# Kernel optimization log

Hardware: AMD Instinct MI355X
Metric: run time of the kernel (lower is better)

## Reference

```python
import jax, jax.numpy as jnp
import numpy as np

EPS = 1e-8


def setup_inputs() -> dict:
    key = jax.random.key(0)
    k1, k2 = jax.random.split(key)
    x = jax.random.normal(k1, (32, 16, 4096), dtype=jnp.float32)
    # shapelets param: (in_channels, num_shapelets, shapelets_size)
    shapelets = jax.random.normal(k2, (16, 64, 64), dtype=jnp.float32)
    return {"x": x, "shapelets": shapelets}


def reference(x, shapelets):
    # x: (B, C, L); shapelets: (C, K, S)
    S = shapelets.shape[2]
    C = x.shape[1]
    W = x.shape[2] - S + 1
    # sliding windows, equivalent to torch unfold(2, S, 1): (B, C, W, S)
    idx = jnp.arange(W)[:, None] + jnp.arange(S)[None, :]
    win = x[:, :, idx]
    win = win / jnp.maximum(jnp.linalg.norm(win, axis=3, keepdims=True), EPS)
    sh = shapelets / jnp.maximum(jnp.linalg.norm(shapelets, axis=2, keepdims=True), EPS)
    # pairwise cosine dot, then mean over channels: (B, W, K)
    sim = jnp.einsum('bcws,cks->bwk', win, sh) / C
    # relu then global max over window positions; torch keeps the summed dim -> (B, 1, K)
    out = jnp.max(jax.nn.relu(sim), axis=1)[:, None, :]
    return out
```

## Files before the change

kernel.cpp:

```cpp
#include <hip/hip_runtime.h>

typedef unsigned int u32;
typedef unsigned short u16;
typedef __bf16 bf16x8 __attribute__((ext_vector_type(8)));
typedef float f32x4 __attribute__((ext_vector_type(4)));

static __device__ __forceinline__ u16 f2bf(float f) {
  u32 u = __float_as_uint(f);
  return (u16)((u + 0x7fffu + ((u >> 16) & 1u)) >> 16);
}
static __device__ __forceinline__ float b2f(u16 v) {
  return __uint_as_float(((u32)v) << 16);
}
static __device__ __forceinline__ u32 pk2(u16 lo, u16 hi) {
  return (u32)lo | ((u32)hi << 16);
}

__global__ __launch_bounds__(256) void prep_kernel(const float* __restrict__ sh,
                                                   u16* __restrict__ shn2,
                                                   float* __restrict__ out) {
  if (blockIdx.x == 0) {
    float4 z = {0.f, 0.f, 0.f, 0.f};
    *(float4*)&out[threadIdx.x * 8] = z;
    *(float4*)&out[threadIdx.x * 8 + 4] = z;
  }
  const int s = threadIdx.x & 63;
  const int wv = threadIdx.x >> 6;
  const int row0 = blockIdx.x * 16 + wv * 4;
#pragma unroll
  for (int r = 0; r < 4; ++r) {
    const int row = row0 + r;
    float v = sh[row * 64 + s];
    float ss = v * v;
#pragma unroll
    for (int o = 1; o < 64; o <<= 1) ss += __shfl_xor(ss, o, 64);
    float iw = 1.0f / fmaxf(sqrtf(ss), 1e-8f);
    const int c = row >> 6, k = row & 63;
    const int chunk = c * 8 + (k >> 4) * 2 + (s >> 5);
    const int pos = ((k & 15) + (((s & 31) >> 3) << 4)) * 8 + (s & 7);
    shn2[chunk * 512 + pos] = f2bf(v * iw);
  }
}

#define WT 128
#define CSTRIDE 104
#define SSTRIDE 1672

__global__ __launch_bounds__(256, 4) void main_kernel(const float* __restrict__ x,
                                                      const u16* __restrict__ shn2,
                                                      float* __restrict__ out) {
  __shared__ u32 xs[4 * SSTRIDE];
  __shared__ u16 invwb[16 * WT];
  __shared__ int redbuf[64];

  const int tid = threadIdx.x;
  const int lane = tid & 63;
  const int wid = tid >> 6;
  const int w0 = blockIdx.x * WT;
  const int b = blockIdx.y;
  const float* xb = x + (size_t)b * 16 * 4096;

  if (tid < 64) redbuf[tid] = 0;

  {
    const int q = tid & 15;
    const int c = tid >> 4;
    if (q < 12) {
      const float* xc = xb + c * 4096;
      const int e0 = w0 + 16 * q;
      float xv[20];
      if (e0 + 19 < 4096) {
#pragma unroll
        for (int r = 0; r < 5; ++r) *(float4*)&xv[4 * r] = *(const float4*)&xc[e0 + 4 * r];
      } else {
#pragma unroll
        for (int j = 0; j < 20; ++j) {
          int g = e0 + j;
          xv[j] = xc[g < 4096 ? g : 4095];
        }
      }
      u16 bf[20];
#pragma unroll
      for (int j = 0; j < 20; ++j) bf[j] = f2bf(xv[j]);
#pragma unroll
      for (int s = 0; s < 4; ++s) {
        u32 pk[8];
#pragma unroll
        for (int r = 0; r < 8; ++r) pk[r] = pk2(bf[2 * r + s], bf[2 * r + s + 1]);
        u32* dst = &xs[s * SSTRIDE + c * CSTRIDE + 8 * q];
        *(uint4*)dst = make_uint4(pk[0], pk[1], pk[2], pk[3]);
        *(uint4*)(dst + 4) = make_uint4(pk[4], pk[5], pk[6], pk[7]);
      }
    }
  }

  {
    const int c = tid >> 4;
    const int wb = (tid & 15) * 8;
    const float* xc = xb + c * 4096;
    const int e0 = w0 + wb;
    float hd[8], tl[8], ss = 0.f;
    if (e0 + 71 < 4096) {
#pragma unroll
      for (int r = 0; r < 16; ++r) {
        float4 v = *(const float4*)&xc[e0 + 4 * r];
        if (r < 2) {
          hd[4 * r + 0] = v.x; hd[4 * r + 1] = v.y;
          hd[4 * r + 2] = v.z; hd[4 * r + 3] = v.w;
        }
        ss += v.x * v.x + v.y * v.y + v.z * v.z + v.w * v.w;
      }
#pragma unroll
      for (int r = 0; r < 2; ++r) {
        float4 v = *(const float4*)&xc[e0 + 64 + 4 * r];
        tl[4 * r + 0] = v.x; tl[4 * r + 1] = v.y;
        tl[4 * r + 2] = v.z; tl[4 * r + 3] = v.w;
      }
    } else {
#pragma unroll
      for (int j = 0; j < 72; ++j) {
        int g = e0 + j;
        float v = xc[g < 4096 ? g : 4095];
        if (j < 8) hd[j] = v;
        if (j >= 64) tl[j - 64] = v;
        if (j < 64) ss += v * v;
      }
    }
    u16 ov[8];
#pragma unroll
    for (int i = 0; i < 8; ++i) {
      float iw = 0.0625f / fmaxf(sqrtf(fmaxf(ss, 0.f)), 1e-8f);
      ov[i] = (e0 + i < 4033) ? f2bf(iw) : (u16)0;
      ss += tl[i] * tl[i] - hd[i] * hd[i];
    }
    *(uint4*)&invwb[c * WT + wb] = make_uint4(pk2(ov[0], ov[1]), pk2(ov[2], ov[3]),
                                              pk2(ov[4], ov[5]), pk2(ov[6], ov[7]));
  }

  __syncthreads();

  f32x4 acc[4][2];
#pragma unroll
  for (int mt = 0; mt < 4; ++mt)
#pragma unroll
    for (int nt = 0; nt < 2; ++nt) acc[mt][nt] = (f32x4){0.f, 0.f, 0.f, 0.f};

  const int m = lane & 15;
  const int h = lane >> 4;
  const int wgrp = wid >> 1;
  const int kgrp = wid & 1;
  const u32* xbase = xs + (m & 3) * SSTRIDE;
  const int joff = 32 * wgrp + 2 * (m >> 2) + 4 * h;
  const u16* shb = shn2 + lane * 8 + kgrp * 4 * 512;
  const int iwbase = 64 * wgrp + 4 * h;

#pragma unroll 2
  for (int c = 0; c < 16; ++c) {
    const u32* xc = xbase + c * CSTRIDE;
    bf16x8 af[6];
#pragma unroll
    for (int f = 0; f < 6; ++f) {
      const u32* p = xc + joff + 8 * f;
      uint2 lo = *(const uint2*)p;
      uint2 hi = *(const uint2*)(p + 2);
      af[f] = __builtin_bit_cast(bf16x8, make_uint4(lo.x, lo.y, hi.x, hi.y));
    }
    const u16* sc = shb + c * 4096;
    bf16x8 bfr[2][2];
#pragma unroll
    for (int nt = 0; nt < 2; ++nt)
#pragma unroll
      for (int ks = 0; ks < 2; ++ks)
        bfr[nt][ks] = __builtin_bit_cast(bf16x8, *(const uint4*)(sc + (nt * 2 + ks) * 512));

#pragma unroll
    for (int mt = 0; mt < 4; ++mt) {
      ushort4 r4 = *(const ushort4*)&invwb[c * WT + iwbase + 16 * mt];
      f32x4 iw = {b2f(r4.x), b2f(r4.y), b2f(r4.z), b2f(r4.w)};
#pragma unroll
      for (int nt = 0; nt < 2; ++nt) {
        f32x4 d = {0.f, 0.f, 0.f, 0.f};
        d = __builtin_amdgcn_mfma_f32_16x16x32_bf16(af[mt],     bfr[nt][0], d, 0, 0, 0);
        d = __builtin_amdgcn_mfma_f32_16x16x32_bf16(af[mt + 2], bfr[nt][1], d, 0, 0, 0);
        acc[mt][nt] += iw * d;
      }
    }
  }

#pragma unroll
  for (int nt = 0; nt < 2; ++nt) {
    float v = 0.f;
#pragma unroll
    for (int mt = 0; mt < 4; ++mt)
      v = fmaxf(v, fmaxf(fmaxf(acc[mt][nt].x, acc[mt][nt].y),
                         fmaxf(acc[mt][nt].z, acc[mt][nt].w)));
    v = fmaxf(v, __shfl_xor(v, 16, 64));
    v = fmaxf(v, __shfl_xor(v, 32, 64));
    if (lane < 16) atomicMax(&redbuf[kgrp * 32 + nt * 16 + lane], __float_as_int(v));
  }
  __syncthreads();
  if (tid < 64) atomicMax((int*)&out[b * 64 + tid], redbuf[tid]);
}

extern "C" void kernel_launch(void* const* d_in, const int* in_sizes, int n_in,
                              void* d_out, int out_size, void* d_ws, size_t ws_size,
                              hipStream_t stream) {
  const float* x = (const float*)d_in[0];
  const float* sh = (const float*)d_in[1];
  float* out = (float*)d_out;
  u16* shn2 = (u16*)d_ws;

  prep_kernel<<<dim3(64), dim3(256), 0, stream>>>(sh, shn2, out);
  main_kernel<<<dim3(32, 32), dim3(256), 0, stream>>>(x, shn2, out);
}
```

Baseline: 45.03 us.

## Double window tile per block and give each wave all 64 shapelets

Each block now covers 256 window positions instead of 128, and each wave computes all 64 shapelets over its 64 windows rather than splitting shapelets across two waves. This halves the grid and the redundant halo loads and norm work per window, and it reuses the A fragments across four N tiles. The cost is twice the accumulator registers, a larger LDS footprint, lower occupancy (launch bounds 3) and fewer blocks, 512 of them across the GPU's compute units.

```diff
diff --git a/kernel.cpp b/kernel.cpp
--- a/kernel.cpp
+++ b/kernel.cpp
@@ -42,15 +42,16 @@
   }
 }
 
-#define WT 128
-#define CSTRIDE 104
-#define SSTRIDE 1672
-
-__global__ __launch_bounds__(256, 4) void main_kernel(const float* __restrict__ x,
+#define WT 256
+#define CSTRIDE 168
+#define SSTRIDE 2696
+#define IWS 264
+
+__global__ __launch_bounds__(256, 3) void main_kernel(const float* __restrict__ x,
                                                       const u16* __restrict__ shn2,
                                                       float* __restrict__ out) {
   __shared__ u32 xs[4 * SSTRIDE];
-  __shared__ u16 invwb[16 * WT];
+  __shared__ u16 invwb[16 * IWS];
   __shared__ int redbuf[64];
 
   const int tid = threadIdx.x;
@@ -63,96 +64,97 @@
   if (tid < 64) redbuf[tid] = 0;
 
   {
+    const int c = tid >> 4;
     const int q = tid & 15;
-    const int c = tid >> 4;
-    if (q < 12) {
-      const float* xc = xb + c * 4096;
-      const int e0 = w0 + 16 * q;
-      float xv[20];
-      if (e0 + 19 < 4096) {
-#pragma unroll
-        for (int r = 0; r < 5; ++r) *(float4*)&xv[4 * r] = *(const float4*)&xc[e0 + 4 * r];
-      } else {
-#pragma unroll
-        for (int j = 0; j < 20; ++j) {
-          int g = e0 + j;
-          xv[j] = xc[g < 4096 ? g : 4095];
-        }
-      }
-      u16 bf[20];
-#pragma unroll
-      for (int j = 0; j < 20; ++j) bf[j] = f2bf(xv[j]);
-#pragma unroll
-      for (int s = 0; s < 4; ++s) {
-        u32 pk[8];
-#pragma unroll
-        for (int r = 0; r < 8; ++r) pk[r] = pk2(bf[2 * r + s], bf[2 * r + s + 1]);
-        u32* dst = &xs[s * SSTRIDE + c * CSTRIDE + 8 * q];
-        *(uint4*)dst = make_uint4(pk[0], pk[1], pk[2], pk[3]);
-        *(uint4*)(dst + 4) = make_uint4(pk[4], pk[5], pk[6], pk[7]);
+    const float* xc = xb + c * 4096;
+    const int e0 = w0 + 20 * q;
+    float xv[24];
+    if (e0 + 23 < 4096) {
+#pragma unroll
+      for (int r = 0; r < 6; ++r) *(float4*)&xv[4 * r] = *(const float4*)&xc[e0 + 4 * r];
+    } else {
+#pragma unroll
+      for (int j = 0; j < 24; ++j) {
+        int g = e0 + j;
+        xv[j] = xc[g < 4096 ? g : 4095];
+      }
+    }
+    u16 bf[24];
+#pragma unroll
+    for (int j = 0; j < 24; ++j) bf[j] = f2bf(xv[j]);
+#pragma unroll
+    for (int s = 0; s < 4; ++s) {
+      u32* dst = &xs[s * SSTRIDE + c * CSTRIDE + 10 * q];
+#pragma unroll
+      for (int r = 0; r < 5; ++r) {
+        uint2 v = make_uint2(pk2(bf[4 * r + s], bf[4 * r + s + 1]),
+                             pk2(bf[4 * r + s + 2], bf[4 * r + s + 3]));
+        *(uint2*)(dst + 2 * r) = v;
       }
     }
   }
 
   {
     const int c = tid >> 4;
-    const int wb = (tid & 15) * 8;
+    const int wb = (tid & 15) * 16;
     const float* xc = xb + c * 4096;
     const int e0 = w0 + wb;
-    float hd[8], tl[8], ss = 0.f;
-    if (e0 + 71 < 4096) {
+    float hd[16], tl[16], ss = 0.f;
+    if (e0 + 79 < 4096) {
 #pragma unroll
       for (int r = 0; r < 16; ++r) {
         float4 v = *(const float4*)&xc[e0 + 4 * r];
-        if (r < 2) {
+        if (r < 4) {
           hd[4 * r + 0] = v.x; hd[4 * r + 1] = v.y;
           hd[4 * r + 2] = v.z; hd[4 * r + 3] = v.w;
         }
         ss += v.x * v.x + v.y * v.y + v.z * v.z + v.w * v.w;
       }
 #pragma unroll
-      for (int r = 0; r < 2; ++r) {
+      for (int r = 0; r < 4; ++r) {
         float4 v = *(const float4*)&xc[e0 + 64 + 4 * r];
         tl[4 * r + 0] = v.x; tl[4 * r + 1] = v.y;
         tl[4 * r + 2] = v.z; tl[4 * r + 3] = v.w;
       }
     } else {
 #pragma unroll
-      for (int j = 0; j < 72; ++j) {
+      for (int j = 0; j < 80; ++j) {
         int g = e0 + j;
         float v = xc[g < 4096 ? g : 4095];
-        if (j < 8) hd[j] = v;
+        if (j < 16) hd[j] = v;
         if (j >= 64) tl[j - 64] = v;
         if (j < 64) ss += v * v;
       }
     }
-    u16 ov[8];
-#pragma unroll
-    for (int i = 0; i < 8; ++i) {
+    u16 ov[16];
+#pragma unroll
+    for (int i = 0; i < 16; ++i) {
       float iw = 0.0625f / fmaxf(sqrtf(fmaxf(ss, 0.f)), 1e-8f);
       ov[i] = (e0 + i < 4033) ? f2bf(iw) : (u16)0;
       ss += tl[i] * tl[i] - hd[i] * hd[i];
     }
-    *(uint4*)&invwb[c * WT + wb] = make_uint4(pk2(ov[0], ov[1]), pk2(ov[2], ov[3]),
-                                              pk2(ov[4], ov[5]), pk2(ov[6], ov[7]));
+    u32* dst = (u32*)&invwb[c * IWS + wb];
+    *(uint4*)dst = make_uint4(pk2(ov[0], ov[1]), pk2(ov[2], ov[3]),
+                              pk2(ov[4], ov[5]), pk2(ov[6], ov[7]));
+    *(uint4*)(dst + 4) = make_uint4(pk2(ov[8], ov[9]), pk2(ov[10], ov[11]),
+                                    pk2(ov[12], ov[13]), pk2(ov[14], ov[15]));
   }
 
   __syncthreads();
 
-  f32x4 acc[4][2];
+  f32x4 acc[4][4];
 #pragma unroll
   for (int mt = 0; mt < 4; ++mt)
 #pragma unroll
-    for (int nt = 0; nt < 2; ++nt) acc[mt][nt] = (f32x4){0.f, 0.f, 0.f, 0.f};
+    for (int nt = 0; nt < 4; ++nt) acc[mt][nt] = (f32x4){0.f, 0.f, 0.f, 0.f};
 
   const int m = lane & 15;
   const int h = lane >> 4;
-  const int wgrp = wid >> 1;
-  const int kgrp = wid & 1;
+  const int wgrp = wid;
   const u32* xbase = xs + (m & 3) * SSTRIDE;
   const int joff = 32 * wgrp + 2 * (m >> 2) + 4 * h;
-  const u16* shb = shn2 + lane * 8 + kgrp * 4 * 512;
-  const int iwbase = 64 * wgrp + 4 * h;
+  const u16* shb = shn2 + lane * 8;
+  const int iwoff = 64 * wgrp + 4 * h;
 
 #pragma unroll 2
   for (int c = 0; c < 16; ++c) {
@@ -165,30 +167,29 @@
       uint2 hi = *(const uint2*)(p + 2);
       af[f] = __builtin_bit_cast(bf16x8, make_uint4(lo.x, lo.y, hi.x, hi.y));
     }
+    f32x4 iwq[4];
+#pragma unroll
+    for (int mt = 0; mt < 4; ++mt) {
+      ushort4 r4 = *(const ushort4*)&invwb[c * IWS + iwoff + 16 * mt];
+      iwq[mt] = (f32x4){b2f(r4.x), b2f(r4.y), b2f(r4.z), b2f(r4.w)};
+    }
     const u16* sc = shb + c * 4096;
-    bf16x8 bfr[2][2];
-#pragma unroll
-    for (int nt = 0; nt < 2; ++nt)
-#pragma unroll
-      for (int ks = 0; ks < 2; ++ks)
-        bfr[nt][ks] = __builtin_bit_cast(bf16x8, *(const uint4*)(sc + (nt * 2 + ks) * 512));
-
-#pragma unroll
-    for (int mt = 0; mt < 4; ++mt) {
-      ushort4 r4 = *(const ushort4*)&invwb[c * WT + iwbase + 16 * mt];
-      f32x4 iw = {b2f(r4.x), b2f(r4.y), b2f(r4.z), b2f(r4.w)};
-#pragma unroll
-      for (int nt = 0; nt < 2; ++nt) {
+#pragma unroll
+    for (int nt = 0; nt < 4; ++nt) {
+      bf16x8 b0 = __builtin_bit_cast(bf16x8, *(const uint4*)(sc + (nt * 2 + 0) * 512));
+      bf16x8 b1 = __builtin_bit_cast(bf16x8, *(const uint4*)(sc + (nt * 2 + 1) * 512));
+#pragma unroll
+      for (int mt = 0; mt < 4; ++mt) {
         f32x4 d = {0.f, 0.f, 0.f, 0.f};
-        d = __builtin_amdgcn_mfma_f32_16x16x32_bf16(af[mt],     bfr[nt][0], d, 0, 0, 0);
-        d = __builtin_amdgcn_mfma_f32_16x16x32_bf16(af[mt + 2], bfr[nt][1], d, 0, 0, 0);
-        acc[mt][nt] += iw * d;
-      }
-    }
-  }
-
-#pragma unroll
-  for (int nt = 0; nt < 2; ++nt) {
+        d = __builtin_amdgcn_mfma_f32_16x16x32_bf16(af[mt],     b0, d, 0, 0, 0);
+        d = __builtin_amdgcn_mfma_f32_16x16x32_bf16(af[mt + 2], b1, d, 0, 0, 0);
+        acc[mt][nt] += iwq[mt] * d;
+      }
+    }
+  }
+
+#pragma unroll
+  for (int nt = 0; nt < 4; ++nt) {
     float v = 0.f;
 #pragma unroll
     for (int mt = 0; mt < 4; ++mt)
@@ -196,7 +197,7 @@
                          fmaxf(acc[mt][nt].z, acc[mt][nt].w)));
     v = fmaxf(v, __shfl_xor(v, 16, 64));
     v = fmaxf(v, __shfl_xor(v, 32, 64));
-    if (lane < 16) atomicMax(&redbuf[kgrp * 32 + nt * 16 + lane], __float_as_int(v));
+    if (lane < 16) atomicMax(&redbuf[nt * 16 + lane], __float_as_int(v));
   }
   __syncthreads();
   if (tid < 64) atomicMax((int*)&out[b * 64 + tid], redbuf[tid]);
@@ -211,5 +212,5 @@
   u16* shn2 = (u16*)d_ws;
 
   prep_kernel<<<dim3(64), dim3(256), 0, stream>>>(sh, shn2, out);
-  main_kernel<<<dim3(32, 32), dim3(256), 0, stream>>>(x, shn2, out);
-}
+  main_kernel<<<dim3(16, 32), dim3(256), 0, stream>>>(x, shn2, out);
+}
```

New measurement: 46.92 us. 1.04x slower.

## Use 512-thread blocks with two-phase shifted bf16 window layout

Applied to the files above, without the earlier changes.

Doubles the block to 512 threads (8 waves), with each wave handling 32 window positions instead of 64, so per-wave accumulators are halved. The shared x buffer drops from four shifted copies to two (pair shifts), and A fragments are read as four contiguous u32 per lane. The aim is higher occupancy and less LDS staging per block. In exchange the shifted-copy addressing changes and row reads may hit LDS bank conflicts, and each wave now reloads the same shapelet B fragments for only half the work.

```diff
diff --git a/kernel.cpp b/kernel.cpp
--- a/kernel.cpp
+++ b/kernel.cpp
@@ -44,13 +44,14 @@
 
 #define WT 128
 #define CSTRIDE 104
-#define SSTRIDE 1672
-
-__global__ __launch_bounds__(256, 4) void main_kernel(const float* __restrict__ x,
+#define PSTRIDE 1680
+#define IWS 136
+
+__global__ __launch_bounds__(512, 6) void main_kernel(const float* __restrict__ x,
                                                       const u16* __restrict__ shn2,
                                                       float* __restrict__ out) {
-  __shared__ u32 xs[4 * SSTRIDE];
-  __shared__ u16 invwb[16 * WT];
+  __shared__ u32 xs[2 * PSTRIDE];
+  __shared__ u16 invwb[16 * IWS];
   __shared__ int redbuf[64];
 
   const int tid = threadIdx.x;
@@ -63,85 +64,74 @@
   if (tid < 64) redbuf[tid] = 0;
 
   {
-    const int q = tid & 15;
-    const int c = tid >> 4;
-    if (q < 12) {
+    const int c = tid >> 5;
+    const int q = tid & 31;
+    if (q < 24) {
       const float* xc = xb + c * 4096;
-      const int e0 = w0 + 16 * q;
-      float xv[20];
-      if (e0 + 19 < 4096) {
-#pragma unroll
-        for (int r = 0; r < 5; ++r) *(float4*)&xv[4 * r] = *(const float4*)&xc[e0 + 4 * r];
+      const int e0 = w0 + 8 * q;
+      float xv[12];
+      if (e0 + 11 < 4096) {
+#pragma unroll
+        for (int r = 0; r < 3; ++r) *(float4*)&xv[4 * r] = *(const float4*)&xc[e0 + 4 * r];
       } else {
 #pragma unroll
-        for (int j = 0; j < 20; ++j) {
+        for (int j = 0; j < 12; ++j) {
           int g = e0 + j;
           xv[j] = xc[g < 4096 ? g : 4095];
         }
       }
-      u16 bf[20];
-#pragma unroll
-      for (int j = 0; j < 20; ++j) bf[j] = f2bf(xv[j]);
-#pragma unroll
-      for (int s = 0; s < 4; ++s) {
-        u32 pk[8];
-#pragma unroll
-        for (int r = 0; r < 8; ++r) pk[r] = pk2(bf[2 * r + s], bf[2 * r + s + 1]);
-        u32* dst = &xs[s * SSTRIDE + c * CSTRIDE + 8 * q];
-        *(uint4*)dst = make_uint4(pk[0], pk[1], pk[2], pk[3]);
-        *(uint4*)(dst + 4) = make_uint4(pk[4], pk[5], pk[6], pk[7]);
-      }
+      u16 bf[10];
+#pragma unroll
+      for (int j = 0; j < 10; ++j) bf[j] = f2bf(xv[j]);
+      u32* d0 = &xs[c * CSTRIDE + 4 * q];
+      *(uint4*)d0 = make_uint4(pk2(bf[0], bf[1]), pk2(bf[2], bf[3]),
+                               pk2(bf[4], bf[5]), pk2(bf[6], bf[7]));
+      u32* d1 = d0 + PSTRIDE;
+      *(uint4*)d1 = make_uint4(pk2(bf[1], bf[2]), pk2(bf[3], bf[4]),
+                               pk2(bf[5], bf[6]), pk2(bf[7], bf[8]));
     }
   }
 
   {
-    const int c = tid >> 4;
-    const int wb = (tid & 15) * 8;
+    const int c = tid >> 5;
+    const int wb = (tid & 31) * 4;
     const float* xc = xb + c * 4096;
     const int e0 = w0 + wb;
-    float hd[8], tl[8], ss = 0.f;
-    if (e0 + 71 < 4096) {
+    float hd[4], tl[4], ss = 0.f;
+    if (e0 + 67 < 4096) {
 #pragma unroll
       for (int r = 0; r < 16; ++r) {
         float4 v = *(const float4*)&xc[e0 + 4 * r];
-        if (r < 2) {
-          hd[4 * r + 0] = v.x; hd[4 * r + 1] = v.y;
-          hd[4 * r + 2] = v.z; hd[4 * r + 3] = v.w;
-        }
+        if (r < 1) { hd[0] = v.x; hd[1] = v.y; hd[2] = v.z; hd[3] = v.w; }
         ss += v.x * v.x + v.y * v.y + v.z * v.z + v.w * v.w;
       }
-#pragma unroll
-      for (int r = 0; r < 2; ++r) {
-        float4 v = *(const float4*)&xc[e0 + 64 + 4 * r];
-        tl[4 * r + 0] = v.x; tl[4 * r + 1] = v.y;
-        tl[4 * r + 2] = v.z; tl[4 * r + 3] = v.w;
-      }
+      float4 v = *(const float4*)&xc[e0 + 64];
+      tl[0] = v.x; tl[1] = v.y; tl[2] = v.z; tl[3] = v.w;
     } else {
 #pragma unroll
-      for (int j = 0; j < 72; ++j) {
+      for (int j = 0; j < 68; ++j) {
         int g = e0 + j;
         float v = xc[g < 4096 ? g : 4095];
-        if (j < 8) hd[j] = v;
+        if (j < 4) hd[j] = v;
         if (j >= 64) tl[j - 64] = v;
         if (j < 64) ss += v * v;
       }
     }
-    u16 ov[8];
-#pragma unroll
-    for (int i = 0; i < 8; ++i) {
+    u16 ov[4];
+#pragma unroll
+    for (int i = 0; i < 4; ++i) {
       float iw = 0.0625f / fmaxf(sqrtf(fmaxf(ss, 0.f)), 1e-8f);
       ov[i] = (e0 + i < 4033) ? f2bf(iw) : (u16)0;
       ss += tl[i] * tl[i] - hd[i] * hd[i];
     }
-    *(uint4*)&invwb[c * WT + wb] = make_uint4(pk2(ov[0], ov[1]), pk2(ov[2], ov[3]),
-                                              pk2(ov[4], ov[5]), pk2(ov[6], ov[7]));
+    *(uint2*)&invwb[c * IWS + wb] = make_uint2(pk2(ov[0], ov[1]), pk2(ov[2], ov[3]));
   }
 
   __syncthreads();
 
-  f32x4 acc[4][2];
-#pragma unroll
-  for (int mt = 0; mt < 4; ++mt)
+  f32x4 acc[2][2];
+#pragma unroll
+  for (int mt = 0; mt < 2; ++mt)
 #pragma unroll
     for (int nt = 0; nt < 2; ++nt) acc[mt][nt] = (f32x4){0.f, 0.f, 0.f, 0.f};
 
@@ -149,40 +139,37 @@
   const int h = lane >> 4;
   const int wgrp = wid >> 1;
   const int kgrp = wid & 1;
-  const u32* xbase = xs + (m & 3) * SSTRIDE;
-  const int joff = 32 * wgrp + 2 * (m >> 2) + 4 * h;
-  const u16* shb = shn2 + lane * 8 + kgrp * 4 * 512;
-  const int iwbase = 64 * wgrp + 4 * h;
+  const u32* xbase = xs + (m & 1) * PSTRIDE;
+  const int jp = 16 * wgrp + (m >> 1) + 4 * h;
+  const u16* shb = shn2 + lane * 8 + kgrp * 2 * 1024;
+  const int iwoff = 32 * wgrp + 4 * h;
 
 #pragma unroll 2
   for (int c = 0; c < 16; ++c) {
     const u32* xc = xbase + c * CSTRIDE;
-    bf16x8 af[6];
-#pragma unroll
-    for (int f = 0; f < 6; ++f) {
-      const u32* p = xc + joff + 8 * f;
-      uint2 lo = *(const uint2*)p;
-      uint2 hi = *(const uint2*)(p + 2);
-      af[f] = __builtin_bit_cast(bf16x8, make_uint4(lo.x, lo.y, hi.x, hi.y));
+    bf16x8 af[4];
+#pragma unroll
+    for (int f = 0; f < 4; ++f) {
+      const u32* p = xc + jp + 8 * f;
+      af[f] = __builtin_bit_cast(bf16x8, make_uint4(p[0], p[1], p[2], p[3]));
+    }
+    f32x4 iwq[2];
+#pragma unroll
+    for (int mt = 0; mt < 2; ++mt) {
+      ushort4 r4 = *(const ushort4*)&invwb[c * IWS + iwoff + 16 * mt];
+      iwq[mt] = (f32x4){b2f(r4.x), b2f(r4.y), b2f(r4.z), b2f(r4.w)};
     }
     const u16* sc = shb + c * 4096;
-    bf16x8 bfr[2][2];
-#pragma unroll
-    for (int nt = 0; nt < 2; ++nt)
-#pragma unroll
-      for (int ks = 0; ks < 2; ++ks)
-        bfr[nt][ks] = __builtin_bit_cast(bf16x8, *(const uint4*)(sc + (nt * 2 + ks) * 512));
-
-#pragma unroll
-    for (int mt = 0; mt < 4; ++mt) {
-      ushort4 r4 = *(const ushort4*)&invwb[c * WT + iwbase + 16 * mt];
-      f32x4 iw = {b2f(r4.x), b2f(r4.y), b2f(r4.z), b2f(r4.w)};
-#pragma unroll
-      for (int nt = 0; nt < 2; ++nt) {
+#pragma unroll
+    for (int nt = 0; nt < 2; ++nt) {
+      bf16x8 b0 = __builtin_bit_cast(bf16x8, *(const uint4*)(sc + (nt * 2 + 0) * 512));
+      bf16x8 b1 = __builtin_bit_cast(bf16x8, *(const uint4*)(sc + (nt * 2 + 1) * 512));
+#pragma unroll
+      for (int mt = 0; mt < 2; ++mt) {
         f32x4 d = {0.f, 0.f, 0.f, 0.f};
-        d = __builtin_amdgcn_mfma_f32_16x16x32_bf16(af[mt],     bfr[nt][0], d, 0, 0, 0);
-        d = __builtin_amdgcn_mfma_f32_16x16x32_bf16(af[mt + 2], bfr[nt][1], d, 0, 0, 0);
-        acc[mt][nt] += iw * d;
+        d = __builtin_amdgcn_mfma_f32_16x16x32_bf16(af[mt],     b0, d, 0, 0, 0);
+        d = __builtin_amdgcn_mfma_f32_16x16x32_bf16(af[mt + 2], b1, d, 0, 0, 0);
+        acc[mt][nt] += iwq[mt] * d;
       }
     }
   }
@@ -191,7 +178,7 @@
   for (int nt = 0; nt < 2; ++nt) {
     float v = 0.f;
 #pragma unroll
-    for (int mt = 0; mt < 4; ++mt)
+    for (int mt = 0; mt < 2; ++mt)
       v = fmaxf(v, fmaxf(fmaxf(acc[mt][nt].x, acc[mt][nt].y),
                          fmaxf(acc[mt][nt].z, acc[mt][nt].w)));
     v = fmaxf(v, __shfl_xor(v, 16, 64));
@@ -211,5 +198,5 @@
   u16* shn2 = (u16*)d_ws;
 
   prep_kernel<<<dim3(64), dim3(256), 0, stream>>>(sh, shn2, out);
-  main_kernel<<<dim3(32, 32), dim3(256), 0, stream>>>(x, shn2, out);
-}
+  main_kernel<<<dim3(32, 32), dim3(512), 0, stream>>>(x, shn2, out);
+}
```

New measurement: 48.61 us. 8.0% more time.
